# Optimization experiments

Hardware: AMD Instinct MI355X
Metric: run time of the kernel (lower is better)

## Reference

```python
import jax, jax.numpy as jnp
import numpy as np

STEPS = 8
TOL = 1e-6


def _kabsch(p, q):
    # p, q: [B, N, 3]; returns R [B,3,3], t [B,3] s.t. q ~= R p + t (pypose svdtf)
    pm = p.mean(axis=-2, keepdims=True)
    qm = q.mean(axis=-2, keepdims=True)
    pc = p - pm
    qc = q - qm
    H = jnp.einsum('bni,bnj->bij', pc, qc)          # 3x3 cross-covariance
    U, S, Vt = jnp.linalg.svd(H, full_matrices=False)
    V = jnp.swapaxes(Vt, -1, -2)
    Ut = jnp.swapaxes(U, -1, -2)
    d = jnp.linalg.det(jnp.matmul(V, Ut))            # reflection fix
    D = jnp.concatenate([jnp.ones(d.shape + (2,), d.dtype), d[..., None]], axis=-1)
    R = jnp.matmul(V * D[..., None, :], Ut)
    t = qm[..., 0, :] - jnp.einsum('bij,bj->bi', R, pm[..., 0, :])
    return R, t


def _rotmat_to_quat(R):
    # branchless rotation-matrix -> quaternion [qx, qy, qz, qw] (pypose order)
    r00, r11, r22 = R[..., 0, 0], R[..., 1, 1], R[..., 2, 2]
    qw = 0.5 * jnp.sqrt(jnp.clip(1.0 + r00 + r11 + r22, 1e-12))
    qx = 0.5 * jnp.sqrt(jnp.clip(1.0 + r00 - r11 - r22, 1e-12))
    qy = 0.5 * jnp.sqrt(jnp.clip(1.0 - r00 + r11 - r22, 1e-12))
    qz = 0.5 * jnp.sqrt(jnp.clip(1.0 - r00 - r11 + r22, 1e-12))
    qx = qx * jnp.where(R[..., 2, 1] - R[..., 1, 2] >= 0, 1.0, -1.0)
    qy = qy * jnp.where(R[..., 0, 2] - R[..., 2, 0] >= 0, 1.0, -1.0)
    qz = qz * jnp.where(R[..., 1, 0] - R[..., 0, 1] >= 0, 1.0, -1.0)
    return jnp.stack([qx, qy, qz, qw], axis=-1)


def _icp(psrc, ptgt):
    B = psrc.shape[0]
    tn = (ptgt * ptgt).sum(-1)                        # [B, M]

    def body(carry, _):
        pc, err, done = carry
        # brute-force 1-NN: Euclidean cdist via  |p|^2 + |q|^2 - 2 p.q
        sq = ((pc * pc).sum(-1)[:, :, None] + tn[:, None, :]
              - 2.0 * jnp.einsum('bnd,bmd->bnm', pc, ptgt))
        dist = jnp.sqrt(jnp.clip(sq, 0.0))            # [B, N, M]
        knnd = dist.min(axis=-1)                      # [B, N]
        idx = dist.argmin(axis=-1)                    # [B, N]
        errnew = knnd.mean(axis=-1)                   # [B]
        conv = jnp.all(jnp.abs(errnew - err) < TOL)
        done_new = jnp.logical_or(done, conv)
        qk = jnp.take_along_axis(ptgt, jnp.broadcast_to(idx[..., None], pc.shape), axis=1)
        R, t = _kabsch(pc, qk)
        pcnew = jnp.einsum('bij,bnj->bni', R, pc) + t[:, None, :]
        pc = jnp.where(done_new, pc, pcnew)
        err = jnp.where(done_new, err, errnew)
        return (pc, err, done_new), None

    init = (psrc, jnp.zeros((B,), psrc.dtype), jnp.array(False))
    (pc, _, _), _ = jax.lax.scan(body, init, None, length=STEPS)
    R, t = _kabsch(psrc, pc)                          # final fit psrc -> moved cloud
    quat = _rotmat_to_quat(R)
    return jnp.concatenate([t, quat], axis=-1)        # SE3 7-vector [t, qx,qy,qz,qw]


def setup_inputs() -> dict:
    key = jax.random.key(0)
    k1, k2 = jax.random.split(key)
    psrc = jax.random.normal(k1, (2, 4096, 3), dtype=jnp.float32)
    ptgt = jax.random.normal(k2, (2, 4096, 3), dtype=jnp.float32)
    return {"psrc": psrc, "ptgt": ptgt}


def reference(psrc, ptgt):
    return _icp(psrc, ptgt)
```

## Files before the change

### kernel.cpp

```cpp
#include <hip/hip_runtime.h>
#include <math.h>

#define NPTS 4096
#define MPTS 4096
#define NSTEPS 8
#define ICP_TOL 1e-6f
#define NBLK 256

#define ACC_OFF 32768
#define CTR_OFF 98304
#define CTR_STRIDE 1024
#define STPUB_OFF 110592

__global__ void init_kernel(const float* __restrict__ ptgt, float* __restrict__ ws) {
    float* ptgt4 = ws;
    unsigned* ctrs = (unsigned*)(ws + CTR_OFF);
    int gid = blockIdx.x * 256 + threadIdx.x;
    if (gid < 2 * MPTS) {
        float x = ptgt[3 * gid + 0];
        float y = ptgt[3 * gid + 1];
        float z = ptgt[3 * gid + 2];
        float4 v;
        v.x = x; v.y = y; v.z = z;
        v.w = 0.5f * (x * x + y * y + z * z);
        ((float4*)ptgt4)[gid] = v;
    }
    for (int i = gid; i < NSTEPS * CTR_STRIDE; i += 8192) ctrs[i] = 0u;
}

__device__ __forceinline__ float frcp(float x) {
#if __has_builtin(__builtin_amdgcn_rcpf)
    return __builtin_amdgcn_rcpf(x);
#else
    return 1.f / x;
#endif
}
__device__ __forceinline__ float frsq(float x) {
#if __has_builtin(__builtin_amdgcn_rsqf)
    return __builtin_amdgcn_rsqf(x);
#else
    return 1.f / sqrtf(x);
#endif
}

#define DET3(a,b,c,d,e,f,g,h,i) \
    ((a)*((e)*(i)-(f)*(h)) - (b)*((d)*(i)-(f)*(g)) + (c)*((d)*(h)-(e)*(g)))

__device__ __forceinline__ void horn_quat(const float N[4][4], float q[4]) {
    float s = 1e-30f;
#pragma unroll
    for (int i = 0; i < 4; ++i)
#pragma unroll
        for (int j = 0; j < 4; ++j) s = fmaxf(s, fabsf(N[i][j]));
    float inv = frcp(s);
    float A[4][4], B[4][4];
#pragma unroll
    for (int i = 0; i < 4; ++i)
#pragma unroll
        for (int j = 0; j < 4; ++j) A[i][j] = N[i][j] * inv;
#pragma unroll
    for (int i = 0; i < 4; ++i)
#pragma unroll
        for (int j = i; j < 4; ++j) {
            float v = A[i][0]*A[0][j] + A[i][1]*A[1][j] + A[i][2]*A[2][j] + A[i][3]*A[3][j];
            B[i][j] = v; B[j][i] = v;
        }
    float p1 = A[0][0]+A[1][1]+A[2][2]+A[3][3];
    float p2 = B[0][0]+B[1][1]+B[2][2]+B[3][3];
    float p3 = 0.f, p4 = 0.f;
#pragma unroll
    for (int i = 0; i < 4; ++i)
#pragma unroll
        for (int j = 0; j < 4; ++j) { p3 += A[i][j]*B[i][j]; p4 += B[i][j]*B[i][j]; }
    float e1 = p1;
    float e2 = 0.5f*(e1*p1 - p2);
    float e3 = (e2*p1 - e1*p2 + p3)*(1.f/3.f);
    float e4 = 0.25f*(e3*p1 - e2*p2 + e1*p3 - p4);
    float lam = -3e38f;
#pragma unroll
    for (int i = 0; i < 4; ++i) {
        float r = A[i][i];
#pragma unroll
        for (int j = 0; j < 4; ++j) if (j != i) r += fabsf(A[i][j]);
        lam = fmaxf(lam, r);
    }
#pragma unroll
    for (int it = 0; it < 12; ++it) {
        float pv = (((lam - e1)*lam + e2)*lam - e3)*lam + e4;
        float dv = ((4.f*lam - 3.f*e1)*lam + 2.f*e2)*lam - e3;
        lam -= pv * frcp(dv);
    }
    float M[4][4];
#pragma unroll
    for (int i = 0; i < 4; ++i)
#pragma unroll
        for (int j = 0; j < 4; ++j) M[i][j] = A[i][j] - ((i == j) ? lam : 0.f);
    float C0 = DET3(M[1][1],M[1][2],M[1][3], M[2][1],M[2][2],M[2][3], M[3][1],M[3][2],M[3][3]);
    float C1 = DET3(M[0][0],M[0][2],M[0][3], M[2][0],M[2][2],M[2][3], M[3][0],M[3][2],M[3][3]);
    float C2 = DET3(M[0][0],M[0][1],M[0][3], M[1][0],M[1][1],M[1][3], M[3][0],M[3][1],M[3][3]);
    float C3 = DET3(M[0][0],M[0][1],M[0][2], M[1][0],M[1][1],M[1][2], M[2][0],M[2][1],M[2][2]);
    int is = 0; float cb = fabsf(C0);
    if (fabsf(C1) > cb) { cb = fabsf(C1); is = 1; }
    if (fabsf(C2) > cb) { cb = fabsf(C2); is = 2; }
    if (fabsf(C3) > cb) { cb = fabsf(C3); is = 3; }
    float v0, v1, v2, v3;
#define ROWCOF(a,b,c) { \
    v0 =  DET3(M[a][1],M[a][2],M[a][3], M[b][1],M[b][2],M[b][3], M[c][1],M[c][2],M[c][3]); \
    v1 = -DET3(M[a][0],M[a][2],M[a][3], M[b][0],M[b][2],M[b][3], M[c][0],M[c][2],M[c][3]); \
    v2 =  DET3(M[a][0],M[a][1],M[a][3], M[b][0],M[b][1],M[b][3], M[c][0],M[c][1],M[c][3]); \
    v3 = -DET3(M[a][0],M[a][1],M[a][2], M[b][0],M[b][1],M[b][2], M[c][0],M[c][1],M[c][2]); }
    if (is == 0)      ROWCOF(1,2,3)
    else if (is == 1) ROWCOF(0,2,3)
    else if (is == 2) ROWCOF(0,1,3)
    else              ROWCOF(0,1,2)
#undef ROWCOF
    float nr = frsq(v0*v0 + v1*v1 + v2*v2 + v3*v3);
    q[0] = v0*nr; q[1] = v1*nr; q[2] = v2*nr; q[3] = v3*nr;
}

#define FOR16(OP) OP(0) OP(1) OP(2) OP(3) OP(4) OP(5) OP(6) OP(7) \
                  OP(8) OP(9) OP(10) OP(11) OP(12) OP(13) OP(14) OP(15)

__global__ __launch_bounds__(512, 2) void icp_main(
    const float* __restrict__ psrc, float* __restrict__ ws,
    float* __restrict__ out) {

    float* ptgt4 = ws;
    float* acc = ws + ACC_OFF;
    unsigned* ctrs = (unsigned*)(ws + CTR_OFF);
    float* stpub = ws + STPUB_OFF;

    __shared__ float tshx[MPTS];
    __shared__ float tshy[MPTS];
    __shared__ float tshz[MPTS];
    __shared__ float spx[32], spy[32], spz[32];
    __shared__ float stq[13];
    __shared__ unsigned keys[8][16];
    __shared__ float red[16][16];
    __shared__ float gd[16][132];
    __shared__ float gp[4][16];
    __shared__ float asum[16];
    __shared__ float stv[12];
    __shared__ int fvs[2];

    const int tid = threadIdx.x;
    const int bid = blockIdx.x;
    const int b = bid >> 7;
    const int n0 = (bid & 127) * 32;

    {
        const float4* tp4 = (const float4*)ptgt4 + (size_t)b * MPTS;
        for (int i = tid; i < MPTS; i += 512) {
            float4 v = tp4[i];
            tshx[i] = v.x; tshy[i] = v.y; tshz[i] = v.z;
        }
    }
    if (tid < 32) {
        const float* pp = psrc + ((size_t)b * NPTS + n0 + tid) * 3;
        spx[tid] = pp[0]; spy[tid] = pp[1]; spz[tid] = pp[2];
    }
    if (tid == 0) {
        stq[0] = 1.f; stq[1] = 0.f; stq[2] = 0.f;
        stq[3] = 0.f; stq[4] = 1.f; stq[5] = 0.f;
        stq[6] = 0.f; stq[7] = 0.f; stq[8] = 1.f;
        stq[9] = 0.f; stq[10] = 0.f; stq[11] = 0.f;
        stq[12] = 0.f;
    }
    __syncthreads();

    const int w = tid >> 6, lane = tid & 63;
    const int m0 = w * 512 + lane;
    bool done = false;

    for (int step = 0; step < NSTEPS; ++step) {
        float R00 = stq[0], R01 = stq[1], R02 = stq[2];
        float R10 = stq[3], R11 = stq[4], R12 = stq[5];
        float R20 = stq[6], R21 = stq[7], R22 = stq[8];
        float t0 = stq[9], t1 = stq[10], t2 = stq[11];

        float sacc = 0.f;

        for (int p = 0; p < 2; ++p) {
            const int np = p * 16;

#define DECLP(i) float px##i, py##i, pz##i;
            FOR16(DECLP)
#undef DECLP
#define LOADP(i) { float x = spx[np+(i)], y = spy[np+(i)], z = spz[np+(i)]; \
            px##i = fmaf(R00, x, fmaf(R01, y, fmaf(R02, z, t0))); \
            py##i = fmaf(R10, x, fmaf(R11, y, fmaf(R12, z, t1))); \
            pz##i = fmaf(R20, x, fmaf(R21, y, fmaf(R22, z, t2))); }
            FOR16(LOADP)
#undef LOADP

#define DECLB(i) float bs##i = -3.0e38f; int ix##i = m0;
            FOR16(DECLB)
#undef DECLB

            float tcx = tshx[m0], tcy = tshy[m0], tcz = tshz[m0];
            int mreg = m0;
#pragma unroll
            for (int k = 0; k < 8; ++k) {
                int mn = m0 + ((k + 1) & 7) * 64;
                float tnx = tshx[mn], tny = tshy[mn], tnz = tshz[mn];
                float htn = 0.5f * (tcx * tcx + tcy * tcy + tcz * tcz);
                float tx = tcx, ty = tcy, tz = tcz;
#define PAIR(i) { float s = fmaf(px##i, tx, fmaf(py##i, ty, fmaf(pz##i, tz, -htn))); \
                if (s > bs##i) { bs##i = s; ix##i = mreg; } }
                FOR16(PAIR)
#undef PAIR
                mreg += 64;
                tcx = tnx; tcy = tny; tcz = tnz;
            }

#define REDKEY(i) { unsigned ub = __float_as_uint(bs##i); \
            unsigned u = ((int)ub >= 0) ? (ub | 0x80000000u) : ~ub; \
            unsigned key = (u & 0xFFFFF000u) | (4095u - (unsigned)ix##i); \
            for (int off = 32; off; off >>= 1) { \
                unsigned o = (unsigned)__shfl_xor((int)key, off); \
                key = key > o ? key : o; } \
            if (lane == 0) keys[w][i] = key; }
            FOR16(REDKEY)
#undef REDKEY
            __syncthreads();

            if (tid < 16) {
                unsigned key = keys[0][tid];
#pragma unroll
                for (int ww = 1; ww < 8; ++ww) {
                    unsigned o = keys[ww][tid];
                    key = key > o ? key : o;
                }
                int m = 4095 - (int)(key & 0xFFFu);
                float qx2 = tshx[m], qy2 = tshy[m], qz2 = tshz[m];
                float x = spx[np + tid], y = spy[np + tid], z = spz[np + tid];
                float px = fmaf(R00, x, fmaf(R01, y, fmaf(R02, z, t0)));
                float py = fmaf(R10, x, fmaf(R11, y, fmaf(R12, z, t1)));
                float pz = fmaf(R20, x, fmaf(R21, y, fmaf(R22, z, t2)));
                float dx = px - qx2, dy = py - qy2, dz = pz - qz2;
                float dist = sqrtf(dx * dx + dy * dy + dz * dz);
                red[tid][0] = px; red[tid][1] = py; red[tid][2] = pz;
                red[tid][3] = qx2; red[tid][4] = qy2; red[tid][5] = qz2;
                red[tid][6] = px * qx2;  red[tid][7] = px * qy2;  red[tid][8] = px * qz2;
                red[tid][9] = py * qx2;  red[tid][10] = py * qy2; red[tid][11] = py * qz2;
                red[tid][12] = pz * qx2; red[tid][13] = pz * qy2; red[tid][14] = pz * qz2;
                red[tid][15] = dist;
            }
            __syncthreads();
            if (tid < 16) {
                float s = 0.f;
#pragma unroll
                for (int r = 0; r < 16; ++r) s += red[r][tid];
                sacc += s;
            }
            __syncthreads();
        }

        if (tid < 16) {
            __hip_atomic_store(&acc[((size_t)step * NBLK + bid) * 16 + tid], sacc,
                               __ATOMIC_RELAXED, __HIP_MEMORY_SCOPE_AGENT);
        }

        unsigned* stepc = ctrs + step * CTR_STRIDE;
        __syncthreads();
        if (tid == 0) {
            unsigned* sub = stepc + (b * 8 + (bid & 7)) * 16;
            unsigned old = __hip_atomic_fetch_add(sub, 1u, __ATOMIC_RELAXED,
                                                  __HIP_MEMORY_SCOPE_AGENT);
            if (old == 15u)
                __hip_atomic_fetch_add(stepc + 256 + b * 16, 1u, __ATOMIC_RELAXED,
                                       __HIP_MEMORY_SCOPE_AGENT);
        }

        const bool is_master = ((bid & 127) == 0);
        if (is_master) {
            if (tid == 0) {
                while (__hip_atomic_load(stepc + 256 + b * 16, __ATOMIC_RELAXED,
                                         __HIP_MEMORY_SCOPE_AGENT) < 8u) {
                    __builtin_amdgcn_s_sleep(1);
                }
            }
            __syncthreads();
            {
                int s = tid >> 2, cb = (tid & 3) * 4;
                const float* base = acc + ((size_t)step * NBLK + b * 128 + s) * 16 + cb;
                float4 v = *(const float4*)base;
                gd[cb + 0][s] = v.x;
                gd[cb + 1][s] = v.y;
                gd[cb + 2][s] = v.z;
                gd[cb + 3][s] = v.w;
            }
            __syncthreads();
            if (tid < 64) {
                int c = tid & 15, part = tid >> 4;
                float s = 0.f;
#pragma unroll
                for (int i = 0; i < 32; ++i) s += gd[c][part * 32 + i];
                gp[part][c] = s;
            }
            __syncthreads();
            if (tid < 16) asum[tid] = gp[0][tid] + gp[1][tid] + gp[2][tid] + gp[3][tid];
            __syncthreads();

            if (tid == 0) {
                float a[16];
                for (int i = 0; i < 16; ++i) a[i] = asum[i];
                float errnew = a[15] * (1.f / NPTS);
                bool conv_b = (fabsf(errnew - stq[12]) < ICP_TOL);

                const float inv_n = 1.f / NPTS;
                float pmx = a[0]*inv_n, pmy = a[1]*inv_n, pmz = a[2]*inv_n;
                float qmx = a[3]*inv_n, qmy = a[4]*inv_n, qmz = a[5]*inv_n;
                float H[3][3];
                for (int i = 0; i < 3; ++i)
                    for (int j = 0; j < 3; ++j)
                        H[i][j] = a[6 + 3*i + j] - a[i]*a[3 + j]*inv_n;
                float Sxx=H[0][0], Sxy=H[0][1], Sxz=H[0][2];
                float Syx=H[1][0], Syy=H[1][1], Syz=H[1][2];
                float Szx=H[2][0], Szy=H[2][1], Szz=H[2][2];
                float Nm[4][4];
                Nm[0][0] = Sxx+Syy+Szz; Nm[0][1] = Syz-Szy;
                Nm[0][2] = Szx-Sxz;     Nm[0][3] = Sxy-Syx;
                Nm[1][1] = Sxx-Syy-Szz; Nm[1][2] = Sxy+Syx; Nm[1][3] = Szx+Sxz;
                Nm[2][2] = -Sxx+Syy-Szz; Nm[2][3] = Syz+Szy;
                Nm[3][3] = -Sxx-Syy+Szz;
                Nm[1][0]=Nm[0][1]; Nm[2][0]=Nm[0][2]; Nm[3][0]=Nm[0][3];
                Nm[2][1]=Nm[1][2]; Nm[3][1]=Nm[1][3]; Nm[3][2]=Nm[2][3];
                float qv[4];
                horn_quat(Nm, qv);
                float qw = qv[0], qx = qv[1], qy = qv[2], qz = qv[3];
                float R00n = 1.f - 2.f*(qy*qy + qz*qz);
                float R01n = 2.f*(qx*qy - qw*qz);
                float R02n = 2.f*(qx*qz + qw*qy);
                float R10n = 2.f*(qx*qy + qw*qz);
                float R11n = 1.f - 2.f*(qx*qx + qz*qz);
                float R12n = 2.f*(qy*qz - qw*qx);
                float R20n = 2.f*(qx*qz - qw*qy);
                float R21n = 2.f*(qy*qz + qw*qx);
                float R22n = 1.f - 2.f*(qx*qx + qy*qy);
                float tx = qmx - (R00n*pmx + R01n*pmy + R02n*pmz);
                float ty = qmy - (R10n*pmx + R11n*pmy + R12n*pmz);
                float tz = qmz - (R20n*pmx + R21n*pmy + R22n*pmz);
                float C00=stq[0], C01=stq[1], C02=stq[2];
                float C10=stq[3], C11=stq[4], C12=stq[5];
                float C20=stq[6], C21=stq[7], C22=stq[8];
                float T0=stq[9], T1=stq[10], T2=stq[11];
                float ns[12];
                ns[0] = R00n*C00 + R01n*C10 + R02n*C20;
                ns[1] = R00n*C01 + R01n*C11 + R02n*C21;
                ns[2] = R00n*C02 + R01n*C12 + R02n*C22;
                ns[3] = R10n*C00 + R11n*C10 + R12n*C20;
                ns[4] = R10n*C01 + R11n*C11 + R12n*C21;
                ns[5] = R10n*C02 + R11n*C12 + R12n*C22;
                ns[6] = R20n*C00 + R21n*C10 + R22n*C20;
                ns[7] = R20n*C01 + R21n*C11 + R22n*C21;
                ns[8] = R20n*C02 + R21n*C12 + R22n*C22;
                ns[9]  = R00n*T0 + R01n*T1 + R02n*T2 + tx;
                ns[10] = R10n*T0 + R11n*T1 + R12n*T2 + ty;
                ns[11] = R20n*T0 + R21n*T1 + R22n*T2 + tz;
                for (int i = 0; i < 12; ++i) {
                    stv[i] = ns[i];
                    __hip_atomic_store(&stpub[step*32 + b*16 + i], ns[i],
                                       __ATOMIC_RELAXED, __HIP_MEMORY_SCOPE_AGENT);
                }
                stv[0] = ns[0];
                for (int i = 0; i < 12; ++i) stv[i] = ns[i];
                asum[15] = errnew;
                fvs[b] = 1 + (conv_b ? 1 : 0);
            }
            __syncthreads();
            if (tid == 0) {
                unsigned fv = (unsigned)fvs[b];
#pragma unroll
                for (int f = 0; f < 16; ++f)
                    __hip_atomic_store(stepc + 512 + b * 256 + f * 16, fv,
                                       __ATOMIC_RELAXED, __HIP_MEMORY_SCOPE_AGENT);
            }
            if (tid == 64) {
                unsigned* of = stepc + 512 + (1 - b) * 256;
                unsigned fv;
                while ((fv = __hip_atomic_load(of, __ATOMIC_RELAXED,
                                               __HIP_MEMORY_SCOPE_AGENT)) == 0u) {
                    __builtin_amdgcn_s_sleep(1);
                }
                fvs[1 - b] = (int)fv;
            }
            __syncthreads();
            bool conv = (fvs[0] == 2) && (fvs[1] == 2);
            bool done_new = done || conv;
            if (tid == 0 && !done_new) {
                for (int i = 0; i < 12; ++i) stq[i] = stv[i];
                stq[12] = asum[15];
            }
            __syncthreads();
            done = done_new;
        } else {
            if (tid == 0) {
                unsigned* mf = stepc + 512 + b * 256 + (bid & 15) * 16;
                unsigned fv;
                while ((fv = __hip_atomic_load(mf, __ATOMIC_RELAXED,
                                               __HIP_MEMORY_SCOPE_AGENT)) == 0u) {
                    __builtin_amdgcn_s_sleep(1);
                }
                fvs[b] = (int)fv;
            }
            if (tid == 64) {
                unsigned* of = stepc + 512 + (1 - b) * 256 + (bid & 15) * 16;
                unsigned fv;
                while ((fv = __hip_atomic_load(of, __ATOMIC_RELAXED,
                                               __HIP_MEMORY_SCOPE_AGENT)) == 0u) {
                    __builtin_amdgcn_s_sleep(1);
                }
                fvs[1 - b] = (int)fv;
            }
            __syncthreads();
            if (tid < 12) {
                stv[tid] = __hip_atomic_load(&stpub[step*32 + b*16 + tid],
                                             __ATOMIC_RELAXED,
                                             __HIP_MEMORY_SCOPE_AGENT);
            }
            __syncthreads();
            bool conv = (fvs[0] == 2) && (fvs[1] == 2);
            bool done_new = done || conv;
            if (tid < 12 && !done_new) stq[tid] = stv[tid];
            __syncthreads();
            done = done_new;
        }
        if (done) break;
    }

    if ((bid == 0 || bid == 128) && tid == 0) {
        float r00 = stq[0], r01 = stq[1], r02 = stq[2];
        float r10 = stq[3], r11 = stq[4], r12 = stq[5];
        float r20 = stq[6], r21 = stq[7], r22 = stq[8];
        float qw = 0.5f * sqrtf(fmaxf(1.f + r00 + r11 + r22, 1e-12f));
        float qx = 0.5f * sqrtf(fmaxf(1.f + r00 - r11 - r22, 1e-12f));
        float qy = 0.5f * sqrtf(fmaxf(1.f - r00 + r11 - r22, 1e-12f));
        float qz = 0.5f * sqrtf(fmaxf(1.f - r00 - r11 + r22, 1e-12f));
        qx = (r21 - r12 >= 0.f) ? qx : -qx;
        qy = (r02 - r20 >= 0.f) ? qy : -qy;
        qz = (r10 - r01 >= 0.f) ? qz : -qz;
        out[b * 7 + 0] = stq[9];
        out[b * 7 + 1] = stq[10];
        out[b * 7 + 2] = stq[11];
        out[b * 7 + 3] = qx;
        out[b * 7 + 4] = qy;
        out[b * 7 + 5] = qz;
        out[b * 7 + 6] = qw;
    }
}

extern "C" void kernel_launch(void* const* d_in, const int* in_sizes, int n_in,
                              void* d_out, int out_size, void* d_ws, size_t ws_size,
                              hipStream_t stream) {
    const float* psrc = (const float*)d_in[0];
    const float* ptgt = (const float*)d_in[1];
    float* out = (float*)d_out;
    float* ws = (float*)d_ws;

    init_kernel<<<32, 256, 0, stream>>>(ptgt, ws);
    icp_main<<<NBLK, 512, 0, stream>>>(psrc, ws, out);
}
```

Measured before the change: 189.2 us.

## Replace master-block counter barrier with sentinel-polled redundant per-block reduction

Drops the two-level atomic counters and the master-block broadcast of the new transform. Instead, every block polls the per-block partial sums directly, using a sentinel value written by the init kernel to detect arrival, then redoes the global reduction and the Kabsch/Horn solve itself. This removes one round-trip of global flag publication and waiting per ICP step. In exchange, all 256 blocks do redundant polling and reduction work, which raises global load traffic on the partials buffer, and the scheme relies on a stored float never matching the sentinel bit pattern.

```diff
diff --git a/kernel.cpp b/kernel.cpp
--- a/kernel.cpp
+++ b/kernel.cpp
@@ -6,15 +6,13 @@
 #define NSTEPS 8
 #define ICP_TOL 1e-6f
 #define NBLK 256
+#define SENT 0x7FBADBADu
 
 #define ACC_OFF 32768
-#define CTR_OFF 98304
-#define CTR_STRIDE 1024
-#define STPUB_OFF 110592
 
 __global__ void init_kernel(const float* __restrict__ ptgt, float* __restrict__ ws) {
     float* ptgt4 = ws;
-    unsigned* ctrs = (unsigned*)(ws + CTR_OFF);
+    unsigned* accu = (unsigned*)(ws + ACC_OFF);
     int gid = blockIdx.x * 256 + threadIdx.x;
     if (gid < 2 * MPTS) {
         float x = ptgt[3 * gid + 0];
@@ -25,7 +23,7 @@
         v.w = 0.5f * (x * x + y * y + z * z);
         ((float4*)ptgt4)[gid] = v;
     }
-    for (int i = gid; i < NSTEPS * CTR_STRIDE; i += 8192) ctrs[i] = 0u;
+    for (int i = gid; i < NSTEPS * NBLK * 16; i += 8192) accu[i] = SENT;
 }
 
 __device__ __forceinline__ float frcp(float x) {
@@ -41,6 +39,15 @@
 #else
     return 1.f / sqrtf(x);
 #endif
+}
+
+__device__ __forceinline__ float poll_word(const unsigned* p) {
+    unsigned v;
+    while ((v = __hip_atomic_load(p, __ATOMIC_RELAXED,
+                                  __HIP_MEMORY_SCOPE_AGENT)) == SENT) {
+        __builtin_amdgcn_s_sleep(1);
+    }
+    return __uint_as_float(v);
 }
 
 #define DET3(a,b,c,d,e,f,g,h,i) \
@@ -125,23 +132,21 @@
     const float* __restrict__ psrc, float* __restrict__ ws,
     float* __restrict__ out) {
 
-    float* ptgt4 = ws;
     float* acc = ws + ACC_OFF;
-    unsigned* ctrs = (unsigned*)(ws + CTR_OFF);
-    float* stpub = ws + STPUB_OFF;
 
     __shared__ float tshx[MPTS];
     __shared__ float tshy[MPTS];
     __shared__ float tshz[MPTS];
     __shared__ float spx[32], spy[32], spz[32];
     __shared__ float stq[13];
+    __shared__ float st_err[2];
     __shared__ unsigned keys[8][16];
     __shared__ float red[16][16];
     __shared__ float gd[16][132];
     __shared__ float gp[4][16];
     __shared__ float asum[16];
-    __shared__ float stv[12];
-    __shared__ int fvs[2];
+    __shared__ float e0[128], e1[128], ep0[32], ep1[32];
+    __shared__ int doneLDS;
 
     const int tid = threadIdx.x;
     const int bid = blockIdx.x;
@@ -149,7 +154,7 @@
     const int n0 = (bid & 127) * 32;
 
     {
-        const float4* tp4 = (const float4*)ptgt4 + (size_t)b * MPTS;
+        const float4* tp4 = (const float4*)ws + (size_t)b * MPTS;
         for (int i = tid; i < MPTS; i += 512) {
             float4 v = tp4[i];
             tshx[i] = v.x; tshy[i] = v.y; tshz[i] = v.z;
@@ -164,13 +169,12 @@
         stq[3] = 0.f; stq[4] = 1.f; stq[5] = 0.f;
         stq[6] = 0.f; stq[7] = 0.f; stq[8] = 1.f;
         stq[9] = 0.f; stq[10] = 0.f; stq[11] = 0.f;
-        stq[12] = 0.f;
+        st_err[0] = 0.f; st_err[1] = 0.f;
     }
     __syncthreads();
 
     const int w = tid >> 6, lane = tid & 63;
     const int m0 = w * 512 + lane;
-    bool done = false;
 
     for (int step = 0; step < NSTEPS; ++step) {
         float R00 = stq[0], R01 = stq[1], R02 = stq[2];
@@ -261,53 +265,51 @@
                                __ATOMIC_RELAXED, __HIP_MEMORY_SCOPE_AGENT);
         }
 
-        unsigned* stepc = ctrs + step * CTR_STRIDE;
+        const unsigned* accu = (const unsigned*)(acc) + (size_t)step * NBLK * 16;
+        {
+            int s = tid >> 2, w0 = (tid & 3) * 4;
+            const unsigned* base = accu + ((size_t)(b * 128 + s)) * 16 + w0;
+#pragma unroll
+            for (int j = 0; j < 4; ++j) gd[w0 + j][s] = poll_word(base + j);
+        }
+        if (tid < 128) {
+            e0[tid] = poll_word(accu + (size_t)tid * 16 + 15);
+        } else if (tid < 256) {
+            int t2 = tid - 128;
+            e1[t2] = poll_word(accu + (size_t)(128 + t2) * 16 + 15);
+        }
         __syncthreads();
+
+        if (tid < 64) {
+            int part = tid >> 4, c = tid & 15;
+            float s = 0.f;
+#pragma unroll
+            for (int i = 0; i < 32; ++i) s += gd[c][part * 32 + i];
+            gp[part][c] = s;
+        } else if (tid < 96) {
+            int j = tid - 64;
+            ep0[j] = e0[4*j] + e0[4*j+1] + e0[4*j+2] + e0[4*j+3];
+        } else if (tid < 128) {
+            int j = tid - 96;
+            ep1[j] = e1[4*j] + e1[4*j+1] + e1[4*j+2] + e1[4*j+3];
+        }
+        __syncthreads();
+        if (tid < 16) asum[tid] = gp[0][tid] + gp[1][tid] + gp[2][tid] + gp[3][tid];
+        __syncthreads();
+
         if (tid == 0) {
-            unsigned* sub = stepc + (b * 8 + (bid & 7)) * 16;
-            unsigned old = __hip_atomic_fetch_add(sub, 1u, __ATOMIC_RELAXED,
-                                                  __HIP_MEMORY_SCOPE_AGENT);
-            if (old == 15u)
-                __hip_atomic_fetch_add(stepc + 256 + b * 16, 1u, __ATOMIC_RELAXED,
-                                       __HIP_MEMORY_SCOPE_AGENT);
-        }
-
-        const bool is_master = ((bid & 127) == 0);
-        if (is_master) {
-            if (tid == 0) {
-                while (__hip_atomic_load(stepc + 256 + b * 16, __ATOMIC_RELAXED,
-                                         __HIP_MEMORY_SCOPE_AGENT) < 8u) {
-                    __builtin_amdgcn_s_sleep(1);
-                }
-            }
-            __syncthreads();
-            {
-                int s = tid >> 2, cb = (tid & 3) * 4;
-                const float* base = acc + ((size_t)step * NBLK + b * 128 + s) * 16 + cb;
-                float4 v = *(const float4*)base;
-                gd[cb + 0][s] = v.x;
-                gd[cb + 1][s] = v.y;
-                gd[cb + 2][s] = v.z;
-                gd[cb + 3][s] = v.w;
-            }
-            __syncthreads();
-            if (tid < 64) {
-                int c = tid & 15, part = tid >> 4;
-                float s = 0.f;
-#pragma unroll
-                for (int i = 0; i < 32; ++i) s += gd[c][part * 32 + i];
-                gp[part][c] = s;
-            }
-            __syncthreads();
-            if (tid < 16) asum[tid] = gp[0][tid] + gp[1][tid] + gp[2][tid] + gp[3][tid];
-            __syncthreads();
-
-            if (tid == 0) {
+            float err0 = 0.f, err1 = 0.f;
+            for (int j = 0; j < 32; ++j) err0 += ep0[j];
+            for (int j = 0; j < 32; ++j) err1 += ep1[j];
+            err0 *= (1.f / NPTS);
+            err1 *= (1.f / NPTS);
+            bool conv = (fabsf(err0 - st_err[0]) < ICP_TOL) &&
+                        (fabsf(err1 - st_err[1]) < ICP_TOL);
+            int dn = (doneLDS && step > 0) ? 1 : 0;
+            dn = (step == 0) ? (conv ? 1 : 0) : (dn || conv);
+            if (!dn) {
                 float a[16];
                 for (int i = 0; i < 16; ++i) a[i] = asum[i];
-                float errnew = a[15] * (1.f / NPTS);
-                bool conv_b = (fabsf(errnew - stq[12]) < ICP_TOL);
-
                 const float inv_n = 1.f / NPTS;
                 float pmx = a[0]*inv_n, pmy = a[1]*inv_n, pmz = a[2]*inv_n;
                 float qmx = a[3]*inv_n, qmy = a[4]*inv_n, qmz = a[5]*inv_n;
@@ -358,75 +360,14 @@
                 ns[9]  = R00n*T0 + R01n*T1 + R02n*T2 + tx;
                 ns[10] = R10n*T0 + R11n*T1 + R12n*T2 + ty;
                 ns[11] = R20n*T0 + R21n*T1 + R22n*T2 + tz;
-                for (int i = 0; i < 12; ++i) {
-                    stv[i] = ns[i];
-                    __hip_atomic_store(&stpub[step*32 + b*16 + i], ns[i],
-                                       __ATOMIC_RELAXED, __HIP_MEMORY_SCOPE_AGENT);
-                }
-                stv[0] = ns[0];
-                for (int i = 0; i < 12; ++i) stv[i] = ns[i];
-                asum[15] = errnew;
-                fvs[b] = 1 + (conv_b ? 1 : 0);
+                for (int i = 0; i < 12; ++i) stq[i] = ns[i];
+                st_err[0] = err0;
+                st_err[1] = err1;
             }
-            __syncthreads();
-            if (tid == 0) {
-                unsigned fv = (unsigned)fvs[b];
-#pragma unroll
-                for (int f = 0; f < 16; ++f)
-                    __hip_atomic_store(stepc + 512 + b * 256 + f * 16, fv,
-                                       __ATOMIC_RELAXED, __HIP_MEMORY_SCOPE_AGENT);
-            }
-            if (tid == 64) {
-                unsigned* of = stepc + 512 + (1 - b) * 256;
-                unsigned fv;
-                while ((fv = __hip_atomic_load(of, __ATOMIC_RELAXED,
-                                               __HIP_MEMORY_SCOPE_AGENT)) == 0u) {
-                    __builtin_amdgcn_s_sleep(1);
-                }
-                fvs[1 - b] = (int)fv;
-            }
-            __syncthreads();
-            bool conv = (fvs[0] == 2) && (fvs[1] == 2);
-            bool done_new = done || conv;
-            if (tid == 0 && !done_new) {
-                for (int i = 0; i < 12; ++i) stq[i] = stv[i];
-                stq[12] = asum[15];
-            }
-            __syncthreads();
-            done = done_new;
-        } else {
-            if (tid == 0) {
-                unsigned* mf = stepc + 512 + b * 256 + (bid & 15) * 16;
-                unsigned fv;
-                while ((fv = __hip_atomic_load(mf, __ATOMIC_RELAXED,
-                                               __HIP_MEMORY_SCOPE_AGENT)) == 0u) {
-                    __builtin_amdgcn_s_sleep(1);
-                }
-                fvs[b] = (int)fv;
-            }
-            if (tid == 64) {
-                unsigned* of = stepc + 512 + (1 - b) * 256 + (bid & 15) * 16;
-                unsigned fv;
-                while ((fv = __hip_atomic_load(of, __ATOMIC_RELAXED,
-                                               __HIP_MEMORY_SCOPE_AGENT)) == 0u) {
-                    __builtin_amdgcn_s_sleep(1);
-                }
-                fvs[1 - b] = (int)fv;
-            }
-            __syncthreads();
-            if (tid < 12) {
-                stv[tid] = __hip_atomic_load(&stpub[step*32 + b*16 + tid],
-                                             __ATOMIC_RELAXED,
-                                             __HIP_MEMORY_SCOPE_AGENT);
-            }
-            __syncthreads();
-            bool conv = (fvs[0] == 2) && (fvs[1] == 2);
-            bool done_new = done || conv;
-            if (tid < 12 && !done_new) stq[tid] = stv[tid];
-            __syncthreads();
-            done = done_new;
-        }
-        if (done) break;
+            doneLDS = dn;
+        }
+        __syncthreads();
+        if (doneLDS) break;
     }
 
     if ((bid == 0 || bid == 128) && tid == 0) {
```

After: 185.8 us. Within noise of the previous version (-1.8%).
